# Performance work log

Measured on AMD Instinct MI355X. Metric: run time of the kernel, lower is better.

## Reference

```python
import jax, jax.numpy as jnp
import numpy as np

N, L, HOP = 512, 16, 8  # L // 2


def overlap_and_add(frames, hop):
    # frames: [..., K, L] -> [..., (K-1)*hop + L]
    K, Lf = frames.shape[-2], frames.shape[-1]
    T = (K - 1) * hop + Lf
    idx = (jnp.arange(K)[:, None] * hop + jnp.arange(Lf)[None, :]).reshape(-1)
    flat = frames.reshape(frames.shape[:-2] + (K * Lf,))
    out = jnp.zeros(frames.shape[:-2] + (T,), frames.dtype)
    return out.at[..., idx].add(flat)


def setup_inputs() -> dict:
    key = jax.random.key(0)
    k1, k2, k3 = jax.random.split(key, 3)
    M, C, K = 8, 2, 6000
    inputs = jax.random.normal(k1, (M, N, K), dtype=jnp.float32)
    est_mask = jax.random.uniform(k2, (M, C, N, K), dtype=jnp.float32)
    W = jax.random.normal(k3, (N, L), dtype=jnp.float32) * 0.05
    return {"inputs": inputs, "est_mask": est_mask, "W": W}


def reference(inputs, est_mask, W):
    # masked source spectra: [M, C, N, K]
    masked = inputs[:, None, :, :] * est_mask
    # transpose to [M, C, K, N] and project N -> L (fused in einsum)
    frames = jnp.einsum('mcnk,nl->mckl', masked, W)  # [M, C, K, L]
    # overlap-and-add with hop L // 2 -> [M, C, T]
    return overlap_and_add(frames, HOP)
```

## Files before the change

### kernel.cpp

```cpp
#include <hip/hip_runtime.h>

#define NN   512
#define LL   16
#define HOPP 8
#define MM   8
#define CC   2
#define KK   6000
#define TT   ((KK - 1) * HOPP + LL)

__global__ __launch_bounds__(512, 6) void decoder_fused_kernel(
    const float* __restrict__ inputs,
    const float* __restrict__ est_mask,
    const float* __restrict__ W,
    float* __restrict__ out)
{
    __shared__ float smem[8448];

    const int tid = threadIdx.x;
    const int t   = tid & 63;
    const int q   = tid >> 6;
    const int kb  = blockIdx.x;
    const int m   = blockIdx.y;

    for (int j = tid; j < (NN * LL / 4); j += 512) {
        reinterpret_cast<float4*>(smem)[j] =
            reinterpret_cast<const float4*>(W)[j];
    }
    __syncthreads();

    const int k  = kb * 64 + t;
    const int kc = (k < KK) ? k : (KK - 1);

    const float* pin = inputs   + ((size_t)m * NN + q * 64) * KK + kc;
    const float* pm0 = est_mask + (((size_t)m * CC + 0) * NN + q * 64) * KK + kc;
    const float* pm1 = pm0 + (size_t)NN * KK;

    float acc0[LL], acc1[LL];
    #pragma unroll
    for (int l = 0; l < LL; ++l) { acc0[l] = 0.f; acc1[l] = 0.f; }

    const float* wrow = &smem[q * 64 * LL];

    #pragma unroll 4
    for (int i = 0; i < 64; ++i) {
        const float vin = pin[(size_t)i * KK];
        const float x0  = vin * pm0[(size_t)i * KK];
        const float x1  = vin * pm1[(size_t)i * KK];
        #pragma unroll
        for (int l = 0; l < LL; ++l) {
            const float w = wrow[i * LL + l];
            acc0[l] = fmaf(x0, w, acc0[l]);
            acc1[l] = fmaf(x1, w, acc1[l]);
        }
    }

    __syncthreads();
    #pragma unroll
    for (int act = 4; act >= 1; act >>= 1) {
        if (q >= act && q < 2 * act) {
            float* dst = &smem[((q - act) * 64 + t) * 33];
            #pragma unroll
            for (int l = 0; l < LL; ++l) { dst[l] = acc0[l]; dst[16 + l] = acc1[l]; }
        }
        __syncthreads();
        if (q < act) {
            const float* srcp = &smem[(q * 64 + t) * 33];
            #pragma unroll
            for (int l = 0; l < LL; ++l) { acc0[l] += srcp[l]; acc1[l] += srcp[16 + l]; }
        }
        __syncthreads();
    }

    if (q == 0) {
        float ph0[8], ph1[8];
        #pragma unroll
        for (int j = 0; j < 8; ++j) {
            ph0[j] = __shfl_up(acc0[8 + j], 1);
            ph1[j] = __shfl_up(acc1[8 + j], 1);
        }

        if (k < KK) {
            float* o0 = out + ((size_t)m * CC + 0) * TT;
            float* o1 = out + ((size_t)m * CC + 1) * TT;
            const int ob = 8 * k;

            if (t == 0) {
                #pragma unroll
                for (int j = 0; j < 8; ++j) {
                    atomicAdd(&o0[ob + j], acc0[j]);
                    atomicAdd(&o1[ob + j], acc1[j]);
                }
            } else {
                #pragma unroll
                for (int j = 0; j < 8; ++j) {
                    o0[ob + j] = acc0[j] + ph0[j];
                    o1[ob + j] = acc1[j] + ph1[j];
                }
            }
            if (t == 63 || k == KK - 1) {
                #pragma unroll
                for (int j = 0; j < 8; ++j) {
                    atomicAdd(&o0[ob + 8 + j], acc0[8 + j]);
                    atomicAdd(&o1[ob + 8 + j], acc1[8 + j]);
                }
            }
        }
    }
}

extern "C" void kernel_launch(void* const* d_in, const int* in_sizes, int n_in,
                              void* d_out, int out_size, void* d_ws, size_t ws_size,
                              hipStream_t stream) {
    const float* inputs   = (const float*)d_in[0];
    const float* est_mask = (const float*)d_in[1];
    const float* W        = (const float*)d_in[2];
    float*       out      = (float*)d_out;

    hipMemsetAsync(out, 0, (size_t)out_size * sizeof(float), stream);

    dim3 grid((KK + 63) / 64, MM);
    decoder_fused_kernel<<<grid, 512, 0, stream>>>(inputs, est_mask, W, out);
}
```

Measured before the change: 69.12 us.

## Process two adjacent frames per thread with float2 loads and float4 weight reads

Each thread now computes two consecutive frames using float2 global loads, and reads weights from shared memory as float4 that are reused across four accumulator sets. Blocks cover 94 frames, with 47 active lanes in the epilogue. Overlap-add between the two frames a thread owns is done in registers. The cross-wave reduction is restructured for the doubled accumulators, and launch bounds drop to 4 waves per SIMD to fit the extra registers. Lanes 47-63 load and compute but are discarded, so some load bandwidth is wasted, and lower occupancy may hurt latency hiding.

```diff
diff --git a/kernel.cpp b/kernel.cpp
--- a/kernel.cpp
+++ b/kernel.cpp
@@ -7,14 +7,16 @@
 #define CC   2
 #define KK   6000
 #define TT   ((KK - 1) * HOPP + LL)
+#define KW   94
+#define NACT 47
 
-__global__ __launch_bounds__(512, 6) void decoder_fused_kernel(
+__global__ __launch_bounds__(512, 4) void decoder_fused_kernel(
     const float* __restrict__ inputs,
     const float* __restrict__ est_mask,
     const float* __restrict__ W,
     float* __restrict__ out)
 {
-    __shared__ float smem[8448];
+    __shared__ float smem[8576];
 
     const int tid = threadIdx.x;
     const int t   = tid & 63;
@@ -28,80 +30,140 @@
     }
     __syncthreads();
 
-    const int k  = kb * 64 + t;
-    const int kc = (k < KK) ? k : (KK - 1);
+    const int kA  = kb * KW + 2 * t;
+    const int kAc = (kA < KK - 1) ? kA : (KK - 2);
 
-    const float* pin = inputs   + ((size_t)m * NN + q * 64) * KK + kc;
-    const float* pm0 = est_mask + (((size_t)m * CC + 0) * NN + q * 64) * KK + kc;
-    const float* pm1 = pm0 + (size_t)NN * KK;
+    const float* base_in = inputs   + ((size_t)m * NN + q * 64) * KK + kAc;
+    const float* base_m0 = est_mask + (((size_t)m * CC + 0) * NN + q * 64) * KK + kAc;
+    const float* base_m1 = base_m0 + (size_t)NN * KK;
 
-    float acc0[LL], acc1[LL];
+    float a0A[LL], a0B[LL], a1A[LL], a1B[LL];
     #pragma unroll
-    for (int l = 0; l < LL; ++l) { acc0[l] = 0.f; acc1[l] = 0.f; }
+    for (int l = 0; l < LL; ++l) { a0A[l] = 0.f; a0B[l] = 0.f; a1A[l] = 0.f; a1B[l] = 0.f; }
 
-    const float* wrow = &smem[q * 64 * LL];
+    const float4* wrow4 = reinterpret_cast<const float4*>(&smem[q * 64 * LL]);
 
-    #pragma unroll 4
+    #pragma unroll 2
     for (int i = 0; i < 64; ++i) {
-        const float vin = pin[(size_t)i * KK];
-        const float x0  = vin * pm0[(size_t)i * KK];
-        const float x1  = vin * pm1[(size_t)i * KK];
+        const float2 vin = *reinterpret_cast<const float2*>(base_in + (size_t)i * KK);
+        const float2 vm0 = *reinterpret_cast<const float2*>(base_m0 + (size_t)i * KK);
+        const float2 vm1 = *reinterpret_cast<const float2*>(base_m1 + (size_t)i * KK);
+        const float x0A = vin.x * vm0.x, x0B = vin.y * vm0.y;
+        const float x1A = vin.x * vm1.x, x1B = vin.y * vm1.y;
         #pragma unroll
-        for (int l = 0; l < LL; ++l) {
-            const float w = wrow[i * LL + l];
-            acc0[l] = fmaf(x0, w, acc0[l]);
-            acc1[l] = fmaf(x1, w, acc1[l]);
+        for (int p = 0; p < 4; ++p) {
+            const float4 w  = wrow4[i * 4 + p];
+            const float wl[4] = {w.x, w.y, w.z, w.w};
+            #pragma unroll
+            for (int u = 0; u < 4; ++u) {
+                const int l = p * 4 + u;
+                a0A[l] = fmaf(x0A, wl[u], a0A[l]);
+                a0B[l] = fmaf(x0B, wl[u], a0B[l]);
+                a1A[l] = fmaf(x1A, wl[u], a1A[l]);
+                a1B[l] = fmaf(x1B, wl[u], a1B[l]);
+            }
         }
     }
 
     __syncthreads();
-    #pragma unroll
-    for (int act = 4; act >= 1; act >>= 1) {
-        if (q >= act && q < 2 * act) {
-            float* dst = &smem[((q - act) * 64 + t) * 33];
-            #pragma unroll
-            for (int l = 0; l < LL; ++l) { dst[l] = acc0[l]; dst[16 + l] = acc1[l]; }
+
+    if (q >= 4) {
+        float* dst = &smem[((q - 4) * 64 + t) * 33];
+        #pragma unroll
+        for (int l = 0; l < LL; ++l) { dst[l] = a0A[l]; dst[16 + l] = a0B[l]; }
+    }
+    __syncthreads();
+    if (q < 4) {
+        const float* s = &smem[(q * 64 + t) * 33];
+        #pragma unroll
+        for (int l = 0; l < LL; ++l) { a0A[l] += s[l]; a0B[l] += s[16 + l]; }
+    }
+    __syncthreads();
+    if (q >= 4) {
+        float* dst = &smem[((q - 4) * 64 + t) * 33];
+        #pragma unroll
+        for (int l = 0; l < LL; ++l) { dst[l] = a1A[l]; dst[16 + l] = a1B[l]; }
+    }
+    __syncthreads();
+    if (q < 4) {
+        const float* s = &smem[(q * 64 + t) * 33];
+        #pragma unroll
+        for (int l = 0; l < LL; ++l) { a1A[l] += s[l]; a1B[l] += s[16 + l]; }
+    }
+    __syncthreads();
+    if (q == 2 || q == 3) {
+        float* dst = &smem[((q - 2) * 64 + t) * 67];
+        #pragma unroll
+        for (int l = 0; l < LL; ++l) {
+            dst[l] = a0A[l]; dst[16 + l] = a0B[l];
+            dst[32 + l] = a1A[l]; dst[48 + l] = a1B[l];
         }
-        __syncthreads();
-        if (q < act) {
-            const float* srcp = &smem[(q * 64 + t) * 33];
-            #pragma unroll
-            for (int l = 0; l < LL; ++l) { acc0[l] += srcp[l]; acc1[l] += srcp[16 + l]; }
+    }
+    __syncthreads();
+    if (q < 2) {
+        const float* s = &smem[(q * 64 + t) * 67];
+        #pragma unroll
+        for (int l = 0; l < LL; ++l) {
+            a0A[l] += s[l]; a0B[l] += s[16 + l];
+            a1A[l] += s[32 + l]; a1B[l] += s[48 + l];
         }
-        __syncthreads();
     }
+    __syncthreads();
+    if (q == 1) {
+        float* dst = &smem[t * 67];
+        #pragma unroll
+        for (int l = 0; l < LL; ++l) {
+            dst[l] = a0A[l]; dst[16 + l] = a0B[l];
+            dst[32 + l] = a1A[l]; dst[48 + l] = a1B[l];
+        }
+    }
+    __syncthreads();
 
     if (q == 0) {
+        {
+            const float* s = &smem[t * 67];
+            #pragma unroll
+            for (int l = 0; l < LL; ++l) {
+                a0A[l] += s[l]; a0B[l] += s[16 + l];
+                a1A[l] += s[32 + l]; a1B[l] += s[48 + l];
+            }
+        }
+
         float ph0[8], ph1[8];
         #pragma unroll
         for (int j = 0; j < 8; ++j) {
-            ph0[j] = __shfl_up(acc0[8 + j], 1);
-            ph1[j] = __shfl_up(acc1[8 + j], 1);
+            ph0[j] = __shfl_up(a0B[8 + j], 1);
+            ph1[j] = __shfl_up(a1B[8 + j], 1);
         }
 
-        if (k < KK) {
-            float* o0 = out + ((size_t)m * CC + 0) * TT;
-            float* o1 = out + ((size_t)m * CC + 1) * TT;
-            const int ob = 8 * k;
+        if (t < NACT && kA < KK) {
+            float* o0 = out + ((size_t)m * CC + 0) * TT + 8 * kA;
+            float* o1 = out + ((size_t)m * CC + 1) * TT + 8 * kA;
 
             if (t == 0) {
                 #pragma unroll
                 for (int j = 0; j < 8; ++j) {
-                    atomicAdd(&o0[ob + j], acc0[j]);
-                    atomicAdd(&o1[ob + j], acc1[j]);
+                    atomicAdd(&o0[j], a0A[j]);
+                    atomicAdd(&o1[j], a1A[j]);
                 }
             } else {
                 #pragma unroll
                 for (int j = 0; j < 8; ++j) {
-                    o0[ob + j] = acc0[j] + ph0[j];
-                    o1[ob + j] = acc1[j] + ph1[j];
+                    o0[j] = a0A[j] + ph0[j];
+                    o1[j] = a1A[j] + ph1[j];
                 }
             }
-            if (t == 63 || k == KK - 1) {
+            #pragma unroll
+            for (int j = 0; j < 8; ++j) {
+                o0[8 + j] = a0B[j] + a0A[8 + j];
+                o1[8 + j] = a1B[j] + a1A[8 + j];
+            }
+            const int kB = kA + 1;
+            if (t == NACT - 1 || kB == KK - 1) {
                 #pragma unroll
                 for (int j = 0; j < 8; ++j) {
-                    atomicAdd(&o0[ob + 8 + j], acc0[8 + j]);
-                    atomicAdd(&o1[ob + 8 + j], acc1[8 + j]);
+                    atomicAdd(&o0[16 + j], a0B[8 + j]);
+                    atomicAdd(&o1[16 + j], a1B[8 + j]);
                 }
             }
         }
@@ -118,6 +180,6 @@
 
     hipMemsetAsync(out, 0, (size_t)out_size * sizeof(float), stream);
 
-    dim3 grid((KK + 63) / 64, MM);
+    dim3 grid((KK + KW - 1) / KW, MM);
     decoder_fused_kernel<<<grid, 512, 0, stream>>>(inputs, est_mask, W, out);
 }
```

Measured after the change: 87.35 us. 1.26x slower.

## Stream input tiles into LDS via async global_load_lds double buffering

Applied to the files above, without the earlier changes.

Replaces per-thread strided global loads with direct global-to-LDS DMA (global_load_lds). The three input tensors are loaded in 32-row chunks, double-buffered so the next chunk's loads overlap compute on the current one. W is no longer staged in shared memory and is read per row from global/cache instead. The goal is to hide memory latency and raise achieved bandwidth, in exchange for larger LDS use, lower occupancy (2 blocks per CU) and a barrier per chunk.

```diff
diff --git a/kernel.cpp b/kernel.cpp
--- a/kernel.cpp
+++ b/kernel.cpp
@@ -2,76 +2,135 @@
 
 #define NN   512
 #define LL   16
-#define HOPP 8
 #define MM   8
 #define CC   2
 #define KK   6000
-#define TT   ((KK - 1) * HOPP + LL)
+#define TT   ((KK - 1) * 8 + 16)
+#define KW   64
+#define NCH  32
+#define NC   (NN / NCH)
+#define ROWB (KK * 4)
+#define TENS_B (NCH * KW * 4)
+#define BUF_B  (3 * TENS_B)
 
-__global__ __launch_bounds__(512, 6) void decoder_fused_kernel(
+typedef __attribute__((address_space(3))) void       lds_v;
+typedef __attribute__((address_space(1))) const void glob_v;
+
+__global__ __launch_bounds__(512, 2) void decoder_dma_kernel(
     const float* __restrict__ inputs,
     const float* __restrict__ est_mask,
     const float* __restrict__ W,
     float* __restrict__ out)
 {
-    __shared__ float smem[8448];
+    __shared__ __align__(16) char lds[2 * BUF_B];
 
     const int tid = threadIdx.x;
     const int t   = tid & 63;
-    const int q   = tid >> 6;
+    const int wq  = __builtin_amdgcn_readfirstlane(tid >> 6);
     const int kb  = blockIdx.x;
     const int m   = blockIdx.y;
 
-    for (int j = tid; j < (NN * LL / 4); j += 512) {
-        reinterpret_cast<float4*>(smem)[j] =
-            reinterpret_cast<const float4*>(W)[j];
-    }
-    __syncthreads();
+    const int lane_r = t >> 4;
+    int cb = kb * 256 + (t & 15) * 16;
+    if (cb > ROWB - 16) cb = ROWB - 16;
+    const size_t lane_off = (size_t)lane_r * ROWB + cb;
 
-    const int k  = kb * 64 + t;
-    const int kc = (k < KK) ? k : (KK - 1);
+    const char* tb0 = (const char*)inputs   + (size_t)m * NN * ROWB;
+    const char* tb1 = (const char*)est_mask + (size_t)(m * CC + 0) * NN * ROWB;
+    const char* tb2 = tb1 + (size_t)NN * ROWB;
+    const char* tb[3] = { tb0, tb1, tb2 };
 
-    const float* pin = inputs   + ((size_t)m * NN + q * 64) * KK + kc;
-    const float* pm0 = est_mask + (((size_t)m * CC + 0) * NN + q * 64) * KK + kc;
-    const float* pm1 = pm0 + (size_t)NN * KK;
+    auto issue = [&](int c, int bsel) {
+        char* bb = lds + bsel * BUF_B;
+        #pragma unroll
+        for (int j = 0; j < 3; ++j) {
+            const int idx  = wq * 3 + j;
+            const int tens = idx >> 3;
+            const int g    = idx & 7;
+            const char* gsrc = tb[tens] + (size_t)(c * NCH + g * 4) * ROWB + lane_off;
+            lds_v* ldst = (lds_v*)(bb + tens * TENS_B + g * 1024);
+            __builtin_amdgcn_global_load_lds((glob_v*)gsrc, ldst, 16, 0, 0);
+        }
+    };
 
     float acc0[LL], acc1[LL];
     #pragma unroll
     for (int l = 0; l < LL; ++l) { acc0[l] = 0.f; acc1[l] = 0.f; }
 
-    const float* wrow = &smem[q * 64 * LL];
+    issue(0, 0);
+    __syncthreads();
 
-    #pragma unroll 4
-    for (int i = 0; i < 64; ++i) {
-        const float vin = pin[(size_t)i * KK];
-        const float x0  = vin * pm0[(size_t)i * KK];
-        const float x1  = vin * pm1[(size_t)i * KK];
+    for (int c = 0; c < NC; ++c) {
+        if (c + 1 < NC) issue(c + 1, (c + 1) & 1);
+
+        const float* Lin = (const float*)(lds + (c & 1) * BUF_B);
+        const float* Lm0 = Lin + 2048;
+        const float* Lm1 = Lin + 4096;
+
         #pragma unroll
-        for (int l = 0; l < LL; ++l) {
-            const float w = wrow[i * LL + l];
-            acc0[l] = fmaf(x0, w, acc0[l]);
-            acc1[l] = fmaf(x1, w, acc1[l]);
-        }
-    }
+        for (int rr = 0; rr < 4; ++rr) {
+            const int r = wq * 4 + rr;
+            const int n = c * NCH + r;
+            float wv[LL];
+            *reinterpret_cast<float4*>(&wv[0])  = *(const float4*)(W + n * LL + 0);
+            *reinterpret_cast<float4*>(&wv[4])  = *(const float4*)(W + n * LL + 4);
+            *reinterpret_cast<float4*>(&wv[8])  = *(const float4*)(W + n * LL + 8);
+            *reinterpret_cast<float4*>(&wv[12]) = *(const float4*)(W + n * LL + 12);
 
-    __syncthreads();
-    #pragma unroll
-    for (int act = 4; act >= 1; act >>= 1) {
-        if (q >= act && q < 2 * act) {
-            float* dst = &smem[((q - act) * 64 + t) * 33];
+            const float xin = Lin[r * 64 + t];
+            const float xm0 = Lm0[r * 64 + t];
+            const float xm1 = Lm1[r * 64 + t];
+            const float x0 = xin * xm0;
+            const float x1 = xin * xm1;
             #pragma unroll
-            for (int l = 0; l < LL; ++l) { dst[l] = acc0[l]; dst[16 + l] = acc1[l]; }
-        }
-        __syncthreads();
-        if (q < act) {
-            const float* srcp = &smem[(q * 64 + t) * 33];
-            #pragma unroll
-            for (int l = 0; l < LL; ++l) { acc0[l] += srcp[l]; acc1[l] += srcp[16 + l]; }
+            for (int l = 0; l < LL; ++l) {
+                acc0[l] = fmaf(x0, wv[l], acc0[l]);
+                acc1[l] = fmaf(x1, wv[l], acc1[l]);
+            }
         }
         __syncthreads();
     }
 
-    if (q == 0) {
+    float* sm = (float*)lds;
+    if (wq >= 4) {
+        float* d = &sm[((wq - 4) * 64 + t) * 33];
+        #pragma unroll
+        for (int l = 0; l < LL; ++l) { d[l] = acc0[l]; d[16 + l] = acc1[l]; }
+    }
+    __syncthreads();
+    if (wq < 4) {
+        const float* s = &sm[(wq * 64 + t) * 33];
+        #pragma unroll
+        for (int l = 0; l < LL; ++l) { acc0[l] += s[l]; acc1[l] += s[16 + l]; }
+    }
+    __syncthreads();
+    if (wq == 2 || wq == 3) {
+        float* d = &sm[((wq - 2) * 64 + t) * 33];
+        #pragma unroll
+        for (int l = 0; l < LL; ++l) { d[l] = acc0[l]; d[16 + l] = acc1[l]; }
+    }
+    __syncthreads();
+    if (wq < 2) {
+        const float* s = &sm[(wq * 64 + t) * 33];
+        #pragma unroll
+        for (int l = 0; l < LL; ++l) { acc0[l] += s[l]; acc1[l] += s[16 + l]; }
+    }
+    __syncthreads();
+    if (wq == 1) {
+        float* d = &sm[t * 33];
+        #pragma unroll
+        for (int l = 0; l < LL; ++l) { d[l] = acc0[l]; d[16 + l] = acc1[l]; }
+    }
+    __syncthreads();
+
+    if (wq == 0) {
+        {
+            const float* s = &sm[t * 33];
+            #pragma unroll
+            for (int l = 0; l < LL; ++l) { acc0[l] += s[l]; acc1[l] += s[16 + l]; }
+        }
+
+        const int k = kb * KW + t;
         float ph0[8], ph1[8];
         #pragma unroll
         for (int j = 0; j < 8; ++j) {
@@ -80,28 +139,27 @@
         }
 
         if (k < KK) {
-            float* o0 = out + ((size_t)m * CC + 0) * TT;
-            float* o1 = out + ((size_t)m * CC + 1) * TT;
-            const int ob = 8 * k;
+            float* o0 = out + ((size_t)m * CC + 0) * TT + 8 * k;
+            float* o1 = out + ((size_t)m * CC + 1) * TT + 8 * k;
 
             if (t == 0) {
                 #pragma unroll
                 for (int j = 0; j < 8; ++j) {
-                    atomicAdd(&o0[ob + j], acc0[j]);
-                    atomicAdd(&o1[ob + j], acc1[j]);
+                    atomicAdd(&o0[j], acc0[j]);
+                    atomicAdd(&o1[j], acc1[j]);
                 }
             } else {
                 #pragma unroll
                 for (int j = 0; j < 8; ++j) {
-                    o0[ob + j] = acc0[j] + ph0[j];
-                    o1[ob + j] = acc1[j] + ph1[j];
+                    o0[j] = acc0[j] + ph0[j];
+                    o1[j] = acc1[j] + ph1[j];
                 }
             }
             if (t == 63 || k == KK - 1) {
                 #pragma unroll
                 for (int j = 0; j < 8; ++j) {
-                    atomicAdd(&o0[ob + 8 + j], acc0[8 + j]);
-                    atomicAdd(&o1[ob + 8 + j], acc1[8 + j]);
+                    atomicAdd(&o0[8 + j], acc0[8 + j]);
+                    atomicAdd(&o1[8 + j], acc1[8 + j]);
                 }
             }
         }
@@ -118,6 +176,6 @@
 
     hipMemsetAsync(out, 0, (size_t)out_size * sizeof(float), stream);
 
-    dim3 grid((KK + 63) / 64, MM);
-    decoder_fused_kernel<<<grid, 512, 0, stream>>>(inputs, est_mask, W, out);
+    dim3 grid((KK + KW - 1) / KW, MM);
+    decoder_dma_kernel<<<grid, 512, 0, stream>>>(inputs, est_mask, W, out);
 }
```

Measured after the change: 64.96 us. 6.0% less time.
